# Performance work log

Measured on AMD Instinct MI355X. Metric: run time of the kernel, lower is better.

## Reference

```python
import jax, jax.numpy as jnp
import numpy as np

INV_TEMP = 10.0

def pairwise_distance(x, y):
    # squared L2 distance: [b,n,c],[b,m,c] -> [b,n,m]
    x2 = jnp.sum(x * x, axis=-1, keepdims=True)          # [b,n,1]
    y2 = jnp.sum(y * y, axis=-1)[:, None, :]             # [b,1,m]
    xy = jnp.einsum('bnc,bmc->bnm', x, y)                # [b,n,m]
    return x2 + y2 - 2.0 * xy

def setup_inputs() -> dict:
    key = jax.random.key(0)
    k1, k2, k3 = jax.random.split(key, 3)
    b, n, m, c = 4, 4096, 4096, 32
    x_f = jax.random.normal(k1, (b, n, c), dtype=jnp.float32)
    y_f = jax.random.normal(k2, (b, m, c), dtype=jnp.float32)
    y_c = jax.random.normal(k3, (b, m, 3), dtype=jnp.float32)
    temp_inv = jnp.ones((1,), dtype=jnp.float32) * INV_TEMP
    return {"x_f": x_f, "y_f": y_f, "y_c": y_c, "temp_inv": temp_inv}

def reference(x_f, y_f, y_c, temp_inv):
    # corr_type='soft', st=True (straight-through)
    dist = pairwise_distance(x_f, y_f)                   # [b,n,m]
    y_soft = jax.nn.softmax(-dist * temp_inv[0], axis=2) # [b,n,m]
    index = jnp.argmax(y_soft, axis=2)                   # [b,n]
    y_hard = jax.nn.one_hot(index, y_soft.shape[2], dtype=y_soft.dtype)
    ret = y_hard - jax.lax.stop_gradient(y_soft) + y_soft
    x_corr = jnp.matmul(ret, y_c)                        # [b,n,3]
    return x_corr
```

## Files before the change

### kernel.cpp

```cpp
#include <hip/hip_runtime.h>

#define B 4
#define N 4096
#define M 4096
#define C 32
#define BN (B * N)
#define MS 16

typedef short bf16x8 __attribute__((ext_vector_type(8)));
typedef float f32x4  __attribute__((ext_vector_type(4)));
typedef unsigned int u32x4 __attribute__((ext_vector_type(4)));

#define WS_WI  ((size_t)MS * BN * 4)
#define WS_YHM (WS_WI * 2)
#define WS_YL  (WS_YHM + (size_t)B * M * C * 2 * 2)
#define WS_Y2  (WS_YL + (size_t)B * M * C * 2)

__device__ __forceinline__ float bf16lo(unsigned int u) { return __uint_as_float(u << 16); }
__device__ __forceinline__ float bf16hi(unsigned int u) { return __uint_as_float(u & 0xffff0000u); }

__device__ __forceinline__ void split3(const float f[8], bf16x8& h, bf16x8& m, bf16x8& l) {
    u32x4 hw, mw, lw;
    #pragma unroll
    for (int p = 0; p < 4; ++p) {
        const float f0 = f[2*p], f1 = f[2*p+1];
        const unsigned int h0 = __float_as_uint(f0) & 0xffff0000u;
        const unsigned int h1 = __float_as_uint(f1) & 0xffff0000u;
        hw[p] = h1 | (h0 >> 16);
        const float r0 = f0 - __uint_as_float(h0);
        const float r1 = f1 - __uint_as_float(h1);
        const unsigned int m0 = __float_as_uint(r0) & 0xffff0000u;
        const unsigned int m1 = __float_as_uint(r1) & 0xffff0000u;
        mw[p] = m1 | (m0 >> 16);
        const float s0 = r0 - __uint_as_float(m0);
        const float s1 = r1 - __uint_as_float(m1);
        lw[p] = (__float_as_uint(s1) & 0xffff0000u) | (__float_as_uint(s0) >> 16);
    }
    h = __builtin_bit_cast(bf16x8, hw);
    m = __builtin_bit_cast(bf16x8, mw);
    l = __builtin_bit_cast(bf16x8, lw);
}

__global__ __launch_bounds__(256)
void y_prepass(const void* __restrict__ yptr, const unsigned short* __restrict__ tptr,
               void* __restrict__ ws) {
    if (tptr[0] == 0x4120) return;
    unsigned short* yhm = (unsigned short*)((char*)ws + WS_YHM);
    unsigned short* ylp = (unsigned short*)((char*)ws + WS_YL);
    float*          y2  = (float*)((char*)ws + WS_Y2);

    const int gid = blockIdx.x * 256 + threadIdx.x;
    const int row = gid >> 2;
    const int seg = gid & 3;
    const int b   = row >> 12;
    const int m   = row & 4095;
    const int chunk = m >> 8;
    const int mr    = m & 255;
    const int mt    = mr >> 4;
    const int colr  = mr & 15;
    const int segs  = seg ^ ((colr >> 1) & 3);
    const float* p = (const float*)yptr + (size_t)row * C + seg * 8;
    float4 v0 = *(const float4*)p;
    float4 v1 = *(const float4*)(p + 4);
    const float f[8] = {v0.x, v0.y, v0.z, v0.w, v1.x, v1.y, v1.z, v1.w};

    bf16x8 h, m_, l;
    split3(f, h, m_, l);
    const size_t hmbase = (size_t)(b * 16 + chunk) * 16384 + mt * 512 + colr * 32 + segs * 8;
    *(bf16x8*)(yhm + hmbase)        = h;
    *(bf16x8*)(yhm + hmbase + 8192) = m_;
    *(bf16x8*)(ylp + (size_t)row * C + seg * 8) = l;

    float s = 0.f;
    #pragma unroll
    for (int k = 0; k < 8; ++k) s = fmaf(f[k], f[k], s);
    s += __shfl_xor(s, 1, 64);
    s += __shfl_xor(s, 2, 64);
    if (seg == 0) y2[row] = -0.5f * s;
}

__global__ __launch_bounds__(256, 4)
void nn_main(const void* __restrict__ xptr, const void* __restrict__ yptr,
             const unsigned short* __restrict__ tptr, void* __restrict__ ws) {
    float* wD = (float*)ws;
    int*   wI = (int*)((char*)ws + WS_WI);
    const bool is_bf16 = (tptr[0] == 0x4120);

    __shared__ uint4 bpl[2048];
    __shared__ float y2s[256];

    const int tid  = threadIdx.x;
    const int lane = tid & 63;
    const int wv   = tid >> 6;
    const int col  = lane & 15;
    const int quad = lane >> 4;
    const int bi   = blockIdx.x;
    const int ms   = bi & 15;
    const int nb   = (bi >> 4) & 15;
    const int b    = bi >> 8;
    const int n_base = nb * 256 + wv * 64;
    const int m0   = ms * 256;

    float bD[4][4];
    int   bI[4][4];
    #pragma unroll
    for (int t = 0; t < 4; ++t)
        #pragma unroll
        for (int r = 0; r < 4; ++r) { bD[t][r] = -__builtin_inff(); bI[t][r] = 0; }

    if (is_bf16) {
        const unsigned short* yp = (const unsigned short*)yptr;
        const unsigned short* xp = (const unsigned short*)xptr;

        {
            const int r = tid;
            const uint4* p = (const uint4*)(yp + ((size_t)b * M + m0 + r) * C);
            float s = 0.f;
            #pragma unroll
            for (int i = 0; i < 4; ++i) {
                uint4 v = p[i];
                float f;
                f = bf16lo(v.x); s = fmaf(f, f, s); f = bf16hi(v.x); s = fmaf(f, f, s);
                f = bf16lo(v.y); s = fmaf(f, f, s); f = bf16hi(v.y); s = fmaf(f, f, s);
                f = bf16lo(v.z); s = fmaf(f, f, s); f = bf16hi(v.z); s = fmaf(f, f, s);
                f = bf16lo(v.w); s = fmaf(f, f, s); f = bf16hi(v.w); s = fmaf(f, f, s);
            }
            y2s[r] = -0.5f * s;
        }

        bf16x8 af[4];
        #pragma unroll
        for (int t = 0; t < 4; ++t)
            af[t] = *(const bf16x8*)(xp + ((size_t)b * N + n_base + t * 16 + col) * C + quad * 8);

        __syncthreads();

        const unsigned short* yb = yp + ((size_t)b * M + m0) * C;
        const size_t boff = (size_t)col * C + quad * 8;
        bf16x8 bfr = *(const bf16x8*)(yb + boff);
        for (int mt = 0; mt < 16; ++mt) {
            bf16x8 bnx = bfr;
            if (mt < 15) bnx = *(const bf16x8*)(yb + boff + (size_t)(mt + 1) * (16 * C));
            const float y2c  = y2s[mt * 16 + col];
            const int   mcur = m0 + mt * 16 + col;
            #pragma unroll
            for (int t = 0; t < 4; ++t) {
                f32x4 acc = {y2c, y2c, y2c, y2c};
                acc = __builtin_amdgcn_mfma_f32_16x16x32_bf16(af[t], bfr, acc, 0, 0, 0);
                #pragma unroll
                for (int r = 0; r < 4; ++r)
                    if (acc[r] > bD[t][r]) { bD[t][r] = acc[r]; bI[t][r] = mcur; }
            }
            bfr = bnx;
        }
    } else {
        const uint4* src = (const uint4*)((char*)ws + WS_YHM + (size_t)(b * 16 + ms) * 32768);
        const float* y2g = (const float*)((char*)ws + WS_Y2) + (size_t)b * M + m0;
        const unsigned short* ylb = (const unsigned short*)((char*)ws + WS_YL) + ((size_t)b * M + m0) * C;

        #pragma unroll
        for (int i = 0; i < 8; ++i) bpl[tid + i * 256] = src[tid + i * 256];
        y2s[tid] = y2g[tid];

        const float* xp = (const float*)xptr;
        bf16x8 ah[4], am[4], al[4];
        #pragma unroll
        for (int t = 0; t < 4; ++t) {
            const float* xr = xp + ((size_t)b * N + n_base + t * 16 + col) * C + quad * 8;
            float4 v0 = *(const float4*)xr;
            float4 v1 = *(const float4*)(xr + 4);
            const float xf[8] = {v0.x, v0.y, v0.z, v0.w, v1.x, v1.y, v1.z, v1.w};
            split3(xf, ah[t], am[t], al[t]);
        }

        __syncthreads();

        const unsigned short* lds = (const unsigned short*)bpl;
        const int fo   = col * 32 + (quad ^ ((col >> 1) & 3)) * 8;
        const size_t lo = (size_t)col * C + quad * 8;

        bf16x8 bh  = *(const bf16x8*)(lds + fo);
        bf16x8 bmi = *(const bf16x8*)(lds + 8192 + fo);
        bf16x8 bl  = *(const bf16x8*)(ylb + lo);
        for (int mt = 0; mt < 16; ++mt) {
            bf16x8 nh = bh, nm = bmi, nl = bl;
            if (mt < 15) {
                const int no = fo + (mt + 1) * 512;
                nh = *(const bf16x8*)(lds + no);
                nm = *(const bf16x8*)(lds + 8192 + no);
                nl = *(const bf16x8*)(ylb + lo + (size_t)(mt + 1) * 512);
            }
            const float y2c  = y2s[mt * 16 + col];
            const int   mcur = m0 + mt * 16 + col;
            #pragma unroll
            for (int t = 0; t < 4; ++t) {
                f32x4 acc = {y2c, y2c, y2c, y2c};
                acc = __builtin_amdgcn_mfma_f32_16x16x32_bf16(am[t], bmi, acc, 0, 0, 0);
                acc = __builtin_amdgcn_mfma_f32_16x16x32_bf16(ah[t], bl,  acc, 0, 0, 0);
                acc = __builtin_amdgcn_mfma_f32_16x16x32_bf16(al[t], bh,  acc, 0, 0, 0);
                acc = __builtin_amdgcn_mfma_f32_16x16x32_bf16(ah[t], bmi, acc, 0, 0, 0);
                acc = __builtin_amdgcn_mfma_f32_16x16x32_bf16(am[t], bh,  acc, 0, 0, 0);
                acc = __builtin_amdgcn_mfma_f32_16x16x32_bf16(ah[t], bh,  acc, 0, 0, 0);
                #pragma unroll
                for (int r = 0; r < 4; ++r)
                    if (acc[r] > bD[t][r]) { bD[t][r] = acc[r]; bI[t][r] = mcur; }
            }
            bh = nh; bmi = nm; bl = nl;
        }
    }

    #pragma unroll
    for (int mask = 1; mask < 16; mask <<= 1) {
        #pragma unroll
        for (int t = 0; t < 4; ++t)
            #pragma unroll
            for (int r = 0; r < 4; ++r) {
                float oD = __shfl_xor(bD[t][r], mask, 64);
                int   oI = __shfl_xor(bI[t][r], mask, 64);
                if (oD > bD[t][r] || (oD == bD[t][r] && oI < bI[t][r])) {
                    bD[t][r] = oD; bI[t][r] = oI;
                }
            }
    }

    if (col == 0) {
        #pragma unroll
        for (int t = 0; t < 4; ++t)
            #pragma unroll
            for (int r = 0; r < 4; ++r) {
                const int n = n_base + t * 16 + quad * 4 + r;
                const size_t g = (size_t)ms * BN + (size_t)b * N + n;
                wD[g] = bD[t][r];
                wI[g] = bI[t][r];
            }
    }
}

__global__ __launch_bounds__(256)
void nn_combine(const float* __restrict__ wD, const int* __restrict__ wI,
                const void* __restrict__ ycptr,
                const unsigned short* __restrict__ tptr,
                void* __restrict__ outptr) {
    const bool is_bf16 = (tptr[0] == 0x4120);
    const int tid  = threadIdx.x;
    const int lane = tid & 63;
    const int wv   = tid >> 6;
    const int s    = lane >> 2;
    const int ro   = lane & 3;
    const int row  = blockIdx.x * 16 + wv * 4 + ro;

    float k  = wD[(size_t)s * BN + row];
    int   ix = wI[(size_t)s * BN + row];
    #pragma unroll
    for (int mask = 4; mask < 64; mask <<= 1) {
        float ok = __shfl_xor(k, mask, 64);
        int   oi = __shfl_xor(ix, mask, 64);
        if (ok > k || (ok == k && oi < ix)) { k = ok; ix = oi; }
    }

    if (s == 0) {
        const int b = row >> 12;
        const size_t src = ((size_t)b * M + ix) * 3;
        if (is_bf16) {
            const unsigned short* yc = (const unsigned short*)ycptr;
            unsigned short* o = (unsigned short*)outptr;
            o[row*3+0] = yc[src+0];
            o[row*3+1] = yc[src+1];
            o[row*3+2] = yc[src+2];
        } else {
            const float* yc = (const float*)ycptr;
            float* o = (float*)outptr;
            o[row*3+0] = yc[src+0];
            o[row*3+1] = yc[src+1];
            o[row*3+2] = yc[src+2];
        }
    }
}

extern "C" void kernel_launch(void* const* d_in, const int* in_sizes, int n_in,
                              void* d_out, int out_size, void* d_ws, size_t ws_size,
                              hipStream_t stream) {
    const void* x  = d_in[0];
    const void* y  = d_in[1];
    const void* yc = d_in[2];
    const unsigned short* t = (const unsigned short*)d_in[3];

    float* wD = (float*)d_ws;
    int*   wI = (int*)((char*)d_ws + WS_WI);

    y_prepass<<<256, 256, 0, stream>>>(y, t, d_ws);
    nn_main<<<1024, 256, 0, stream>>>(x, y, t, d_ws);
    nn_combine<<<1024, 256, 0, stream>>>(wD, wI, yc, t, d_out);
}
```

Baseline: 92.60 us.

## Split y prepass across twice the threads and remap nn_main block order

The y prepass now gives each thread four floats instead of eight, doubling the grid to 512 blocks and adding one more shuffle step for the row norm, so more waves are available to hide memory latency. nn_main's block index is remapped so that consecutive blocks cover eight m-chunks for the same n-block, which changes which x/y tiles run concurrently and how well they hit in L2. In exchange, the prepass issues smaller 8-byte stores and does more index math per element.

```diff
diff --git a/kernel.cpp b/kernel.cpp
--- a/kernel.cpp
+++ b/kernel.cpp
@@ -10,6 +10,7 @@
 typedef short bf16x8 __attribute__((ext_vector_type(8)));
 typedef float f32x4  __attribute__((ext_vector_type(4)));
 typedef unsigned int u32x4 __attribute__((ext_vector_type(4)));
+typedef unsigned int u32x2 __attribute__((ext_vector_type(2)));
 
 #define WS_WI  ((size_t)MS * BN * 4)
 #define WS_YHM (WS_WI * 2)
@@ -41,6 +42,24 @@
     l = __builtin_bit_cast(bf16x8, lw);
 }
 
+__device__ __forceinline__ void split3_4(const float f[4], u32x2& h, u32x2& m, u32x2& l) {
+    #pragma unroll
+    for (int p = 0; p < 2; ++p) {
+        const float f0 = f[2*p], f1 = f[2*p+1];
+        const unsigned int h0 = __float_as_uint(f0) & 0xffff0000u;
+        const unsigned int h1 = __float_as_uint(f1) & 0xffff0000u;
+        h[p] = h1 | (h0 >> 16);
+        const float r0 = f0 - __uint_as_float(h0);
+        const float r1 = f1 - __uint_as_float(h1);
+        const unsigned int m0 = __float_as_uint(r0) & 0xffff0000u;
+        const unsigned int m1 = __float_as_uint(r1) & 0xffff0000u;
+        m[p] = m1 | (m0 >> 16);
+        const float s0 = r0 - __uint_as_float(m0);
+        const float s1 = r1 - __uint_as_float(m1);
+        l[p] = (__float_as_uint(s1) & 0xffff0000u) | (__float_as_uint(s0) >> 16);
+    }
+}
+
 __global__ __launch_bounds__(256)
 void y_prepass(const void* __restrict__ yptr, const unsigned short* __restrict__ tptr,
                void* __restrict__ ws) {
@@ -49,34 +68,37 @@
     unsigned short* ylp = (unsigned short*)((char*)ws + WS_YL);
     float*          y2  = (float*)((char*)ws + WS_Y2);
 
-    const int gid = blockIdx.x * 256 + threadIdx.x;
-    const int row = gid >> 2;
-    const int seg = gid & 3;
-    const int b   = row >> 12;
-    const int m   = row & 4095;
+    const int gid  = blockIdx.x * 256 + threadIdx.x;
+    const int row  = gid >> 3;
+    const int hs   = gid & 7;
+    const int seg  = hs >> 1;
+    const int half = hs & 1;
+    const int b    = row >> 12;
+    const int m    = row & 4095;
     const int chunk = m >> 8;
     const int mr    = m & 255;
     const int mt    = mr >> 4;
     const int colr  = mr & 15;
     const int segs  = seg ^ ((colr >> 1) & 3);
-    const float* p = (const float*)yptr + (size_t)row * C + seg * 8;
-    float4 v0 = *(const float4*)p;
-    float4 v1 = *(const float4*)(p + 4);
-    const float f[8] = {v0.x, v0.y, v0.z, v0.w, v1.x, v1.y, v1.z, v1.w};
-
-    bf16x8 h, m_, l;
-    split3(f, h, m_, l);
-    const size_t hmbase = (size_t)(b * 16 + chunk) * 16384 + mt * 512 + colr * 32 + segs * 8;
-    *(bf16x8*)(yhm + hmbase)        = h;
-    *(bf16x8*)(yhm + hmbase + 8192) = m_;
-    *(bf16x8*)(ylp + (size_t)row * C + seg * 8) = l;
+
+    const float* p = (const float*)yptr + (size_t)row * C + seg * 8 + half * 4;
+    float4 v = *(const float4*)p;
+    const float f[4] = {v.x, v.y, v.z, v.w};
+
+    u32x2 h, m_, l;
+    split3_4(f, h, m_, l);
+    const size_t hmbase = (size_t)(b * 16 + chunk) * 16384 + mt * 512 + colr * 32 + segs * 8 + half * 4;
+    *(u32x2*)(yhm + hmbase)        = h;
+    *(u32x2*)(yhm + hmbase + 8192) = m_;
+    *(u32x2*)(ylp + (size_t)row * C + seg * 8 + half * 4) = l;
 
     float s = 0.f;
     #pragma unroll
-    for (int k = 0; k < 8; ++k) s = fmaf(f[k], f[k], s);
+    for (int k = 0; k < 4; ++k) s = fmaf(f[k], f[k], s);
     s += __shfl_xor(s, 1, 64);
     s += __shfl_xor(s, 2, 64);
-    if (seg == 0) y2[row] = -0.5f * s;
+    s += __shfl_xor(s, 4, 64);
+    if (hs == 0) y2[row] = -0.5f * s;
 }
 
 __global__ __launch_bounds__(256, 4)
@@ -95,9 +117,10 @@
     const int col  = lane & 15;
     const int quad = lane >> 4;
     const int bi   = blockIdx.x;
-    const int ms   = bi & 15;
-    const int nb   = (bi >> 4) & 15;
-    const int b    = bi >> 8;
+    const int nb   = (bi >> 3) & 15;
+    const int g    = (bi & 7) + ((bi >> 7) << 3);
+    const int ms   = g & 15;
+    const int b    = g >> 4;
     const int n_base = nb * 256 + wv * 64;
     const int m0   = ms * 256;
 
@@ -229,9 +252,9 @@
             #pragma unroll
             for (int r = 0; r < 4; ++r) {
                 const int n = n_base + t * 16 + quad * 4 + r;
-                const size_t g = (size_t)ms * BN + (size_t)b * N + n;
-                wD[g] = bD[t][r];
-                wI[g] = bI[t][r];
+                const size_t gidx = (size_t)ms * BN + (size_t)b * N + n;
+                wD[gidx] = bD[t][r];
+                wI[gidx] = bI[t][r];
             }
     }
 }
@@ -288,7 +311,7 @@
     float* wD = (float*)d_ws;
     int*   wI = (int*)((char*)d_ws + WS_WI);
 
-    y_prepass<<<256, 256, 0, stream>>>(y, t, d_ws);
+    y_prepass<<<512, 256, 0, stream>>>(y, t, d_ws);
     nn_main<<<1024, 256, 0, stream>>>(x, y, t, d_ws);
     nn_combine<<<1024, 256, 0, stream>>>(wD, wI, yc, t, d_out);
 }
```

Measured after the change: 92.59 us. Within noise of the previous version (-0.0%).
